# Kernel tuning notes

Hardware: AMD Instinct MI355X
Metric: run time of the kernel (lower is better)

Reference implementation:

```python
import jax, jax.numpy as jnp
import numpy as np
import math

B, S, E, H, D = 2, 2048, 1024, 16, 64

def setup_inputs() -> dict:
    key = jax.random.key(0)
    ks = jax.random.split(key, 9)
    sc = 0.02
    return {
        "x": jax.random.normal(ks[0], (B, S, E), jnp.float32),
        "Wq": jax.random.normal(ks[1], (H, E, D), jnp.float32) * sc,
        "Wk": jax.random.normal(ks[2], (H, E, D), jnp.float32) * sc,
        "Wv": jax.random.normal(ks[3], (H, E, D), jnp.float32) * sc,
        "bq": jax.random.normal(ks[4], (H, D), jnp.float32) * sc,
        "bk": jax.random.normal(ks[5], (H, D), jnp.float32) * sc,
        "bv": jax.random.normal(ks[6], (H, D), jnp.float32) * sc,
        "Wo": jax.random.normal(ks[7], (H * D, E), jnp.float32) * sc,
        "bo": jax.random.normal(ks[8], (E,), jnp.float32) * sc,
    }

def reference(x, Wq, Wk, Wv, bq, bk, bv, Wo, bo):
    # per-head projections, batched over heads: [B,H,S,D]
    q = jnp.einsum('bse,hed->bhsd', x, Wq) + bq[None, :, None, :]
    k = jnp.einsum('bse,hed->bhsd', x, Wk) + bk[None, :, None, :]
    v = jnp.einsum('bse,hed->bhsd', x, Wv) + bv[None, :, None, :]
    # full score matrix [B,H,S,S], scaled by sqrt(head_size) as in original
    scores = jnp.einsum('bhqd,bhkd->bhqk', q, k) / math.sqrt(D)
    causal = jnp.tril(jnp.ones((S, S), bool))  # tril mask as in buffer
    scores = jnp.where(causal[None, None], scores, -jnp.inf)
    attn = jax.nn.softmax(scores, axis=-1)
    out = jnp.einsum('bhqk,bhkd->bhqd', attn, v)
    # concat heads in head order: [B,S,H*D]
    out = out.transpose(0, 2, 1, 3).reshape(B, S, H * D)
    # output projection (dropout is identity in eval / p=0)
    return out @ Wo + bo
```

## Files before the change

### kernel.cpp

```cpp
#include <hip/hip_runtime.h>

#define BB 2
#define SS 2048
#define EE 1024
#define HH 16
#define DD 64

typedef unsigned short u16;
typedef float f4 __attribute__((ext_vector_type(4)));
typedef __bf16 b8 __attribute__((ext_vector_type(8)));
typedef short s8i __attribute__((ext_vector_type(8)));
typedef u16 u16x4 __attribute__((ext_vector_type(4)));

__device__ inline u16 f2b(float f) {
  unsigned u = __builtin_bit_cast(unsigned, f);
  unsigned r = (u + 0x7fffu + ((u >> 16) & 1u)) >> 16;
  return (u16)r;
}

__global__ __launch_bounds__(256) void prep(const float* __restrict__ x,
                                            const float* __restrict__ Wq,
                                            const float* __restrict__ Wk,
                                            const float* __restrict__ Wv,
                                            const float* __restrict__ Wo,
                                            u16* __restrict__ xb,
                                            u16* __restrict__ Wt,
                                            u16* __restrict__ Wot) {
  int bid = blockIdx.x;
  int t = threadIdx.x;
  if (bid < 1024) {
    int i0 = bid * 256 + t;
    for (int j = 0; j < 4; ++j) {
      int i = i0 + j * 262144;
      f4 v = ((const f4*)x)[i];
      u16x4 o;
      for (int k2 = 0; k2 < 4; ++k2) o[k2] = f2b(v[k2]);
      ((u16x4*)xb)[i] = o;
    }
  } else if (bid < 1792) {
    __shared__ float tile[64][65];
    int z = bid - 1024;
    int y = z >> 4;
    int e0 = (z & 15) * 64;
    int qkv = y >> 4, h = y & 15;
    const float* W = (qkv == 0) ? Wq : (qkv == 1) ? Wk : Wv;
    for (int p = 0; p < 16; ++p) {
      int i = p * 4 + (t >> 6), d = t & 63;
      tile[i][d] = W[((size_t)h * EE + e0 + i) * DD + d];
    }
    __syncthreads();
    for (int p = 0; p < 16; ++p) {
      int d = p * 4 + (t >> 6), i = t & 63;
      Wt[((size_t)qkv * 1024 + h * 64 + d) * EE + e0 + i] = f2b(tile[i][d]);
    }
  } else {
    __shared__ float tile2[64][65];
    int z = bid - 1792;
    int e0 = (z & 15) * 64, c0 = (z >> 4) * 64;
    for (int p = 0; p < 16; ++p) {
      int i = p * 4 + (t >> 6), j = t & 63;
      tile2[i][j] = Wo[(size_t)(e0 + i) * (HH * DD) + c0 + j];
    }
    __syncthreads();
    for (int p = 0; p < 16; ++p) {
      int j = p * 4 + (t >> 6), i = t & 63;
      Wot[(size_t)(c0 + j) * EE + e0 + i] = f2b(tile2[i][j]);
    }
  }
}

__global__ __launch_bounds__(256) void gemmQKV(
    const u16* __restrict__ xb, const u16* __restrict__ Wt,
    u16* __restrict__ Qo, u16* __restrict__ Ko, u16* __restrict__ Vo,
    const float* __restrict__ bq, const float* __restrict__ bk,
    const float* __restrict__ bv) {
  const int K = 1024;
  __shared__ u16 SM[8192];
  u16* As = SM;
  u16* Bs = SM + 4096;
  int t = threadIdx.x;
  int lane = t & 63, w = t >> 6;
  int wr = w >> 1, wc = w & 1;
  int lr = lane & 15, lg = lane >> 4;

  int bid = blockIdx.x;
  bool isV = bid >= 512;
  int m0, n0;
  const u16 *Ap, *Bp;
  if (!isV) {
    m0 = (bid >> 4) * 128;
    n0 = (bid & 15) * 128;
    Ap = xb;
    Bp = Wt;
  } else {
    int z = bid - 512;
    m0 = (z >> 5) * 128;
    n0 = (z & 31) * 128;
    Ap = Wt + (size_t)2048 * 1024;
    Bp = xb;
  }

  f4 acc[4][4];
  const f4 z4 = {0.f, 0.f, 0.f, 0.f};
  for (int mi = 0; mi < 4; ++mi)
    for (int ni = 0; ni < 4; ++ni) acc[mi][ni] = z4;

  int r0 = t >> 2, s0 = t & 3;
  const u16* ga0 = Ap + (size_t)(m0 + r0) * K + s0 * 8;
  const u16* gb0 = Bp + (size_t)(n0 + r0) * K + s0 * 8;
  u16* la0 = As + w * 512;
  u16* la1 = As + 2048 + w * 512;
  u16* lb0 = Bs + w * 512;
  u16* lb1 = Bs + 2048 + w * 512;

  for (int ks = 0; ks < K / 32; ++ks) {
    int k0 = ks * 32;
    __builtin_amdgcn_global_load_lds(
        (const __attribute__((address_space(1))) void*)(ga0 + k0),
        (__attribute__((address_space(3))) void*)la0, 16, 0, 0);
    __builtin_amdgcn_global_load_lds(
        (const __attribute__((address_space(1))) void*)(ga0 + 64 * K + k0),
        (__attribute__((address_space(3))) void*)la1, 16, 0, 0);
    __builtin_amdgcn_global_load_lds(
        (const __attribute__((address_space(1))) void*)(gb0 + k0),
        (__attribute__((address_space(3))) void*)lb0, 16, 0, 0);
    __builtin_amdgcn_global_load_lds(
        (const __attribute__((address_space(1))) void*)(gb0 + 64 * K + k0),
        (__attribute__((address_space(3))) void*)lb1, 16, 0, 0);
    __syncthreads();
    b8 af[4], bf[4];
    for (int mi = 0; mi < 4; ++mi)
      af[mi] = *(const b8*)&As[(wr * 64 + mi * 16 + lr) * 32 + lg * 8];
    for (int ni = 0; ni < 4; ++ni)
      bf[ni] = *(const b8*)&Bs[(wc * 64 + ni * 16 + lr) * 32 + lg * 8];
    for (int mi = 0; mi < 4; ++mi)
      for (int ni = 0; ni < 4; ++ni)
        acc[mi][ni] = __builtin_amdgcn_mfma_f32_16x16x32_bf16(af[mi], bf[ni],
                                                              acc[mi][ni], 0, 0, 0);
    __syncthreads();
  }

  const float QSC = 0.18033688011112042f;
  u16(*SMv)[128] = (u16(*)[128])SM;
  for (int hh = 0; hh < 2; ++hh) {
    __syncthreads();
    if (wr == hh) {
      for (int mi = 0; mi < 4; ++mi)
        for (int ni = 0; ni < 4; ++ni)
          for (int r = 0; r < 4; ++r) {
            int lrow = mi * 16 + lg * 4 + r;
            int lcol = wc * 64 + ni * 16 + lr;
            float v = acc[mi][ni][r];
            if (!isV) {
              int n_g = n0 + lcol;
              int qkv = n_g >> 10, hd = n_g & 1023;
              v += (qkv == 0) ? bq[hd] : bk[hd];
              if (qkv == 0) v *= QSC;
            } else {
              v += bv[m0 + hh * 64 + lrow];
            }
            SMv[lrow][lcol] = f2b(v);
          }
    }
    __syncthreads();
    if (!isV) {
      int b = m0 >> 11;
      int sbase = (m0 & 2047) + hh * 64;
      for (int q = 0; q < 4; ++q) {
        int c = t + q * 256;
        int h_i = c >> 9, row = (c >> 3) & 63, slot = c & 7;
        int n_g = n0 + h_i * 64;
        int qkv = n_g >> 10, hd = n_g & 1023;
        int h = hd >> 6;
        u16* dst = (qkv == 0) ? Qo : Ko;
        *(s8i*)(dst + (((size_t)b * HH + h) * SS + sbase + row) * DD + slot * 8) =
            *(const s8i*)&SMv[row][h_i * 64 + slot * 8];
      }
    } else {
      int b = n0 >> 11;
      int scol = n0 & 2047;
      int h = (m0 + hh * 64) >> 6;
      int dbase = (m0 + hh * 64) & 63;
      for (int q = 0; q < 4; ++q) {
        int c = t + q * 256;
        int row = c >> 4, slot = c & 15;
        *(s8i*)(Vo + (((size_t)b * HH + h) * DD + dbase + row) * SS + scol + slot * 8) =
            *(const s8i*)&SMv[row][slot * 8];
      }
    }
  }
}

__global__ __launch_bounds__(256) void gemmO(const u16* __restrict__ A,
                                             const u16* __restrict__ Bm,
                                             float* __restrict__ Co,
                                             const float* __restrict__ bo) {
  const int K = 1024;
  __shared__ u16 As[128 * 32];
  __shared__ u16 Bs[64 * 32];
  __shared__ float Sf[64 * 64];
  int t = threadIdx.x;
  int lane = t & 63, w = t >> 6;
  int lr = lane & 15, lg = lane >> 4;
  int m0 = blockIdx.y * 128, n0 = blockIdx.x * 64;

  f4 acc[2][4];
  const f4 z4 = {0.f, 0.f, 0.f, 0.f};
  for (int mi = 0; mi < 2; ++mi)
    for (int ni = 0; ni < 4; ++ni) acc[mi][ni] = z4;

  int r0 = t >> 2, s0 = t & 3;
  const u16* ga0 = A + (size_t)(m0 + r0) * K + s0 * 8;
  const u16* gb0 = Bm + (size_t)(n0 + r0) * K + s0 * 8;
  u16* la0 = As + w * 512;
  u16* la1 = As + 2048 + w * 512;
  u16* lb0 = Bs + w * 512;

  for (int ks = 0; ks < K / 32; ++ks) {
    int k0 = ks * 32;
    __builtin_amdgcn_global_load_lds(
        (const __attribute__((address_space(1))) void*)(ga0 + k0),
        (__attribute__((address_space(3))) void*)la0, 16, 0, 0);
    __builtin_amdgcn_global_load_lds(
        (const __attribute__((address_space(1))) void*)(ga0 + 64 * K + k0),
        (__attribute__((address_space(3))) void*)la1, 16, 0, 0);
    __builtin_amdgcn_global_load_lds(
        (const __attribute__((address_space(1))) void*)(gb0 + k0),
        (__attribute__((address_space(3))) void*)lb0, 16, 0, 0);
    __syncthreads();
    b8 af[2], bf[4];
    for (int mi = 0; mi < 2; ++mi)
      af[mi] = *(const b8*)&As[(w * 32 + mi * 16 + lr) * 32 + lg * 8];
    for (int ni = 0; ni < 4; ++ni)
      bf[ni] = *(const b8*)&Bs[(ni * 16 + lr) * 32 + lg * 8];
    for (int mi = 0; mi < 2; ++mi)
      for (int ni = 0; ni < 4; ++ni)
        acc[mi][ni] = __builtin_amdgcn_mfma_f32_16x16x32_bf16(af[mi], bf[ni],
                                                              acc[mi][ni], 0, 0, 0);
    __syncthreads();
  }

  for (int hh = 0; hh < 2; ++hh) {
    __syncthreads();
    if ((w >> 1) == hh) {
      for (int mi = 0; mi < 2; ++mi)
        for (int ni = 0; ni < 4; ++ni)
          for (int r = 0; r < 4; ++r) {
            int lrow = (w & 1) * 32 + mi * 16 + lg * 4 + r;
            int lcol = ni * 16 + lr;
            Sf[lrow * 64 + lcol] = acc[mi][ni][r] + bo[n0 + lcol];
          }
    }
    __syncthreads();
    for (int q = 0; q < 4; ++q) {
      int c = t + q * 256;
      int row = c >> 4, slot = c & 15;
      *(f4*)(Co + (size_t)(m0 + hh * 64 + row) * 1024 + n0 + slot * 4) =
          *(const f4*)&Sf[row * 64 + slot * 4];
    }
  }
}

#define KST 72
#define PST 72
__global__ __launch_bounds__(256) void fattn(const u16* __restrict__ Qb,
                                             const u16* __restrict__ Kb,
                                             const u16* __restrict__ VTb,
                                             u16* __restrict__ AO) {
  __shared__ u16 Kl[2][64 * KST];
  __shared__ u16 Vl[2][64 * KST];
  __shared__ u16 Pl[4][16 * PST];

  int t = threadIdx.x, lane = t & 63, w = t >> 6;
  int lr = lane & 15, lg = lane >> 4;
  int bh = blockIdx.y;
  int b = bh >> 4, h = bh & 15;
  size_t base = (size_t)bh * SS * DD;

  int r0 = t >> 2, s0 = t & 3;
  u16* kl0 = &Kl[0][r0 * KST + s0 * 8];
  u16* kl1 = &Kl[1][r0 * KST + s0 * 8];
  u16* vl0 = &Vl[0][r0 * KST + s0 * 8];
  u16* vl1 = &Vl[1][r0 * KST + s0 * 8];
  const u16* kg = Kb + base + (size_t)r0 * DD + s0 * 8;
  const u16* vg = VTb + base + (size_t)r0 * SS + s0 * 8;

  for (int half = 0; half < 2; ++half) {
    int qt = half ? blockIdx.x : 31 - blockIdx.x;
    int qbase = qt * 64;
    int nt = qt + 1;

    const u16* qp = Qb + base + (size_t)(qbase + w * 16 + lr) * DD;
    b8 qf0 = *(const b8*)(qp + lg * 8);
    b8 qf1 = *(const b8*)(qp + 32 + lg * 8);

    const f4 z4 = {0.f, 0.f, 0.f, 0.f};
    f4 o[4];
    for (int i = 0; i < 4; ++i) o[i] = z4;
    float mrow[4], lsum[4];
    for (int r = 0; r < 4; ++r) { mrow[r] = -1e30f; lsum[r] = 0.f; }
    int qg = qbase + w * 16 + lg * 4;

    {
      *(s8i*)kl0 = *(const s8i*)(kg);
      *(s8i*)(kl0 + 32) = *(const s8i*)(kg + 32);
      *(s8i*)vl0 = *(const s8i*)(vg);
      *(s8i*)(vl0 + 32) = *(const s8i*)(vg + 32);
    }
    __syncthreads();

    for (int kt = 0; kt < nt; ++kt) {
      int cur = kt & 1;
      int kv0 = kt * 64;

      s8i nk0, nk1, nv0, nv1;
      bool more = (kt + 1 < nt);
      if (more) {
        const u16* kgn = kg + (size_t)(kv0 + 64) * DD;
        const u16* vgn = vg + kv0 + 64;
        nk0 = *(const s8i*)(kgn);
        nk1 = *(const s8i*)(kgn + 32);
        nv0 = *(const s8i*)(vgn);
        nv1 = *(const s8i*)(vgn + 32);
      }

      f4 sa[4];
      for (int n = 0; n < 4; ++n) sa[n] = z4;
      for (int n = 0; n < 4; ++n) {
        b8 kf0 = *(const b8*)&Kl[cur][(n * 16 + lr) * KST + lg * 8];
        b8 kf1 = *(const b8*)&Kl[cur][(n * 16 + lr) * KST + 32 + lg * 8];
        sa[n] = __builtin_amdgcn_mfma_f32_16x16x32_bf16(qf0, kf0, sa[n], 0, 0, 0);
        sa[n] = __builtin_amdgcn_mfma_f32_16x16x32_bf16(qf1, kf1, sa[n], 0, 0, 0);
      }

      if (kt == nt - 1) {
        for (int r = 0; r < 4; ++r) {
          int q = qg + r;
          if (kv0 + lr > q) sa[0][r] = -1e30f;
          if (kv0 + 16 + lr > q) sa[1][r] = -1e30f;
          if (kv0 + 32 + lr > q) sa[2][r] = -1e30f;
          if (kv0 + 48 + lr > q) sa[3][r] = -1e30f;
        }
      }

      float scl[4];
      for (int r = 0; r < 4; ++r) {
        float mx = fmaxf(fmaxf(sa[0][r], sa[1][r]), fmaxf(sa[2][r], sa[3][r]));
        mx = fmaxf(mx, __shfl_xor(mx, 1));
        mx = fmaxf(mx, __shfl_xor(mx, 2));
        mx = fmaxf(mx, __shfl_xor(mx, 4));
        mx = fmaxf(mx, __shfl_xor(mx, 8));
        float mn = fmaxf(mrow[r], mx);
        float sc = __builtin_amdgcn_exp2f(mrow[r] - mn);
        float p0 = __builtin_amdgcn_exp2f(sa[0][r] - mn);
        float p1 = __builtin_amdgcn_exp2f(sa[1][r] - mn);
        float p2 = __builtin_amdgcn_exp2f(sa[2][r] - mn);
        float p3 = __builtin_amdgcn_exp2f(sa[3][r] - mn);
        lsum[r] = lsum[r] * sc + ((p0 + p1) + (p2 + p3));
        mrow[r] = mn;
        scl[r] = sc;
        int prow = (lg * 4 + r) * PST;
        Pl[w][prow + lr] = f2b(p0);
        Pl[w][prow + 16 + lr] = f2b(p1);
        Pl[w][prow + 32 + lr] = f2b(p2);
        Pl[w][prow + 48 + lr] = f2b(p3);
      }
      for (int n = 0; n < 4; ++n) {
        f4 ov = o[n];
        for (int r = 0; r < 4; ++r) ov[r] *= scl[r];
        o[n] = ov;
      }

      b8 pf0 = *(const b8*)&Pl[w][lr * PST + lg * 8];
      b8 pf1 = *(const b8*)&Pl[w][lr * PST + 32 + lg * 8];
      for (int n = 0; n < 4; ++n) {
        b8 vf0 = *(const b8*)&Vl[cur][(n * 16 + lr) * KST + lg * 8];
        b8 vf1 = *(const b8*)&Vl[cur][(n * 16 + lr) * KST + 32 + lg * 8];
        o[n] = __builtin_amdgcn_mfma_f32_16x16x32_bf16(pf0, vf0, o[n], 0, 0, 0);
        o[n] = __builtin_amdgcn_mfma_f32_16x16x32_bf16(pf1, vf1, o[n], 0, 0, 0);
      }

      if (more) {
        u16* kln = cur ? kl0 : kl1;
        u16* vln = cur ? vl0 : vl1;
        *(s8i*)kln = nk0;
        *(s8i*)(kln + 32) = nk1;
        *(s8i*)vln = nv0;
        *(s8i*)(vln + 32) = nv1;
      }
      __syncthreads();
    }

    float rl[4];
    for (int r = 0; r < 4; ++r) {
      float s = lsum[r];
      s += __shfl_xor(s, 1);
      s += __shfl_xor(s, 2);
      s += __shfl_xor(s, 4);
      s += __shfl_xor(s, 8);
      rl[r] = 1.f / s;
    }
    for (int n = 0; n < 4; ++n)
      for (int r = 0; r < 4; ++r) {
        int qgr = qg + r;
        int d = n * 16 + lr;
        AO[((size_t)b * SS + qgr) * (HH * DD) + h * DD + d] = f2b(o[n][r] * rl[r]);
      }
    __syncthreads();
  }
}

extern "C" void kernel_launch(void* const* d_in, const int* in_sizes, int n_in,
                              void* d_out, int out_size, void* d_ws, size_t ws_size,
                              hipStream_t stream) {
  const float* x  = (const float*)d_in[0];
  const float* Wq = (const float*)d_in[1];
  const float* Wk = (const float*)d_in[2];
  const float* Wv = (const float*)d_in[3];
  const float* bq = (const float*)d_in[4];
  const float* bk = (const float*)d_in[5];
  const float* bv = (const float*)d_in[6];
  const float* Wo = (const float*)d_in[7];
  const float* bo = (const float*)d_in[8];

  char* ws = (char*)d_ws;
  u16* xb  = (u16*)(ws);
  u16* Wt  = (u16*)(ws + ((size_t)8 << 20));
  u16* Wot = (u16*)(ws + ((size_t)14 << 20));
  u16* Qw  = (u16*)(ws + ((size_t)16 << 20));
  u16* Kw  = (u16*)(ws + ((size_t)24 << 20));
  u16* VTw = (u16*)(ws + ((size_t)32 << 20));
  u16* AO  = xb;

  prep<<<2048, 256, 0, stream>>>(x, Wq, Wk, Wv, Wo, xb, Wt, Wot);
  gemmQKV<<<768, 256, 0, stream>>>(xb, Wt, Qw, Kw, VTw, bq, bk, bv);
  fattn<<<dim3(16, 32), 256, 0, stream>>>(Qw, Kw, VTw, AO);
  gemmO<<<dim3(16, 32), 256, 0, stream>>>(AO, Wot, (float*)d_out, bo);
}
```

Measured before the change: 237.6 us.

## Use 128-row query tiles with 8 waves and XOR-swizzled K/V shared layout

The flash-attention kernel now uses 512-thread blocks, each handling one 128-query tile with 8 waves. This replaces the previous 4-wave blocks that processed two paired 64-query tiles in sequence. The grid becomes 1D with head-major ordering, and the largest tiles are scheduled first. K/V staging is spread over twice as many threads with one 16-byte load each and an XOR swizzle on column slots to cut LDS bank conflicts. Each K/V tile load is shared by twice as many query rows, at the cost of fewer blocks and masking on the last two tiles.

```diff
diff --git a/kernel.cpp b/kernel.cpp
--- a/kernel.cpp
+++ b/kernel.cpp
@@ -263,151 +263,143 @@
 
 #define KST 72
 #define PST 72
-__global__ __launch_bounds__(256) void fattn(const u16* __restrict__ Qb,
+__global__ __launch_bounds__(512) void fattn(const u16* __restrict__ Qb,
                                              const u16* __restrict__ Kb,
                                              const u16* __restrict__ VTb,
                                              u16* __restrict__ AO) {
   __shared__ u16 Kl[2][64 * KST];
   __shared__ u16 Vl[2][64 * KST];
-  __shared__ u16 Pl[4][16 * PST];
+  __shared__ u16 Pl[8][16 * PST];
 
   int t = threadIdx.x, lane = t & 63, w = t >> 6;
   int lr = lane & 15, lg = lane >> 4;
-  int bh = blockIdx.y;
+  int id = blockIdx.x;
+  int bh = id & 31;
+  int p = id >> 5;
+  int qb = (p < 8) ? (15 - p) : (p - 8);
   int b = bh >> 4, h = bh & 15;
   size_t base = (size_t)bh * SS * DD;
 
-  int r0 = t >> 2, s0 = t & 3;
-  u16* kl0 = &Kl[0][r0 * KST + s0 * 8];
-  u16* kl1 = &Kl[1][r0 * KST + s0 * 8];
-  u16* vl0 = &Vl[0][r0 * KST + s0 * 8];
-  u16* vl1 = &Vl[1][r0 * KST + s0 * 8];
+  int r0 = t >> 3, s0 = t & 7;
+  int s0p = s0 ^ (r0 & 7);
+  u16* kl0 = &Kl[0][r0 * KST + s0p * 8];
+  u16* kl1 = &Kl[1][r0 * KST + s0p * 8];
+  u16* vl0 = &Vl[0][r0 * KST + s0p * 8];
+  u16* vl1 = &Vl[1][r0 * KST + s0p * 8];
   const u16* kg = Kb + base + (size_t)r0 * DD + s0 * 8;
   const u16* vg = VTb + base + (size_t)r0 * SS + s0 * 8;
 
-  for (int half = 0; half < 2; ++half) {
-    int qt = half ? blockIdx.x : 31 - blockIdx.x;
-    int qbase = qt * 64;
-    int nt = qt + 1;
-
-    const u16* qp = Qb + base + (size_t)(qbase + w * 16 + lr) * DD;
-    b8 qf0 = *(const b8*)(qp + lg * 8);
-    b8 qf1 = *(const b8*)(qp + 32 + lg * 8);
-
-    const f4 z4 = {0.f, 0.f, 0.f, 0.f};
-    f4 o[4];
-    for (int i = 0; i < 4; ++i) o[i] = z4;
-    float mrow[4], lsum[4];
-    for (int r = 0; r < 4; ++r) { mrow[r] = -1e30f; lsum[r] = 0.f; }
-    int qg = qbase + w * 16 + lg * 4;
-
-    {
-      *(s8i*)kl0 = *(const s8i*)(kg);
-      *(s8i*)(kl0 + 32) = *(const s8i*)(kg + 32);
-      *(s8i*)vl0 = *(const s8i*)(vg);
-      *(s8i*)(vl0 + 32) = *(const s8i*)(vg + 32);
-    }
-    __syncthreads();
-
-    for (int kt = 0; kt < nt; ++kt) {
-      int cur = kt & 1;
-      int kv0 = kt * 64;
-
-      s8i nk0, nk1, nv0, nv1;
-      bool more = (kt + 1 < nt);
-      if (more) {
-        const u16* kgn = kg + (size_t)(kv0 + 64) * DD;
-        const u16* vgn = vg + kv0 + 64;
-        nk0 = *(const s8i*)(kgn);
-        nk1 = *(const s8i*)(kgn + 32);
-        nv0 = *(const s8i*)(vgn);
-        nv1 = *(const s8i*)(vgn + 32);
+  int qbase = qb * 128;
+  int nt = 2 * qb + 2;
+
+  const u16* qp = Qb + base + (size_t)(qbase + w * 16 + lr) * DD;
+  b8 qf0 = *(const b8*)(qp + lg * 8);
+  b8 qf1 = *(const b8*)(qp + 32 + lg * 8);
+
+  const f4 z4 = {0.f, 0.f, 0.f, 0.f};
+  f4 o[4];
+  for (int i = 0; i < 4; ++i) o[i] = z4;
+  float mrow[4], lsum[4];
+  for (int r = 0; r < 4; ++r) { mrow[r] = -1e30f; lsum[r] = 0.f; }
+  int qg = qbase + w * 16 + lg * 4;
+
+  int fsl = lg ^ (lr & 7);
+
+  *(s8i*)kl0 = *(const s8i*)kg;
+  *(s8i*)vl0 = *(const s8i*)vg;
+  __syncthreads();
+
+  for (int kt = 0; kt < nt; ++kt) {
+    int cur = kt & 1;
+    int kv0 = kt * 64;
+
+    s8i nk, nv;
+    bool more = (kt + 1 < nt);
+    if (more) {
+      nk = *(const s8i*)(kg + (size_t)(kv0 + 64) * DD);
+      nv = *(const s8i*)(vg + kv0 + 64);
+    }
+
+    f4 sa[4];
+    for (int n = 0; n < 4; ++n) sa[n] = z4;
+    for (int n = 0; n < 4; ++n) {
+      const u16* krow = &Kl[cur][(n * 16 + lr) * KST];
+      b8 kf0 = *(const b8*)(krow + fsl * 8);
+      b8 kf1 = *(const b8*)(krow + (fsl ^ 4) * 8);
+      sa[n] = __builtin_amdgcn_mfma_f32_16x16x32_bf16(qf0, kf0, sa[n], 0, 0, 0);
+      sa[n] = __builtin_amdgcn_mfma_f32_16x16x32_bf16(qf1, kf1, sa[n], 0, 0, 0);
+    }
+
+    if (kt >= nt - 2) {
+      for (int r = 0; r < 4; ++r) {
+        int q = qg + r;
+        if (kv0 + lr > q) sa[0][r] = -1e30f;
+        if (kv0 + 16 + lr > q) sa[1][r] = -1e30f;
+        if (kv0 + 32 + lr > q) sa[2][r] = -1e30f;
+        if (kv0 + 48 + lr > q) sa[3][r] = -1e30f;
       }
-
-      f4 sa[4];
-      for (int n = 0; n < 4; ++n) sa[n] = z4;
-      for (int n = 0; n < 4; ++n) {
-        b8 kf0 = *(const b8*)&Kl[cur][(n * 16 + lr) * KST + lg * 8];
-        b8 kf1 = *(const b8*)&Kl[cur][(n * 16 + lr) * KST + 32 + lg * 8];
-        sa[n] = __builtin_amdgcn_mfma_f32_16x16x32_bf16(qf0, kf0, sa[n], 0, 0, 0);
-        sa[n] = __builtin_amdgcn_mfma_f32_16x16x32_bf16(qf1, kf1, sa[n], 0, 0, 0);
-      }
-
-      if (kt == nt - 1) {
-        for (int r = 0; r < 4; ++r) {
-          int q = qg + r;
-          if (kv0 + lr > q) sa[0][r] = -1e30f;
-          if (kv0 + 16 + lr > q) sa[1][r] = -1e30f;
-          if (kv0 + 32 + lr > q) sa[2][r] = -1e30f;
-          if (kv0 + 48 + lr > q) sa[3][r] = -1e30f;
-        }
-      }
-
-      float scl[4];
-      for (int r = 0; r < 4; ++r) {
-        float mx = fmaxf(fmaxf(sa[0][r], sa[1][r]), fmaxf(sa[2][r], sa[3][r]));
-        mx = fmaxf(mx, __shfl_xor(mx, 1));
-        mx = fmaxf(mx, __shfl_xor(mx, 2));
-        mx = fmaxf(mx, __shfl_xor(mx, 4));
-        mx = fmaxf(mx, __shfl_xor(mx, 8));
-        float mn = fmaxf(mrow[r], mx);
-        float sc = __builtin_amdgcn_exp2f(mrow[r] - mn);
-        float p0 = __builtin_amdgcn_exp2f(sa[0][r] - mn);
-        float p1 = __builtin_amdgcn_exp2f(sa[1][r] - mn);
-        float p2 = __builtin_amdgcn_exp2f(sa[2][r] - mn);
-        float p3 = __builtin_amdgcn_exp2f(sa[3][r] - mn);
-        lsum[r] = lsum[r] * sc + ((p0 + p1) + (p2 + p3));
-        mrow[r] = mn;
-        scl[r] = sc;
-        int prow = (lg * 4 + r) * PST;
-        Pl[w][prow + lr] = f2b(p0);
-        Pl[w][prow + 16 + lr] = f2b(p1);
-        Pl[w][prow + 32 + lr] = f2b(p2);
-        Pl[w][prow + 48 + lr] = f2b(p3);
-      }
-      for (int n = 0; n < 4; ++n) {
-        f4 ov = o[n];
-        for (int r = 0; r < 4; ++r) ov[r] *= scl[r];
-        o[n] = ov;
-      }
-
-      b8 pf0 = *(const b8*)&Pl[w][lr * PST + lg * 8];
-      b8 pf1 = *(const b8*)&Pl[w][lr * PST + 32 + lg * 8];
-      for (int n = 0; n < 4; ++n) {
-        b8 vf0 = *(const b8*)&Vl[cur][(n * 16 + lr) * KST + lg * 8];
-        b8 vf1 = *(const b8*)&Vl[cur][(n * 16 + lr) * KST + 32 + lg * 8];
-        o[n] = __builtin_amdgcn_mfma_f32_16x16x32_bf16(pf0, vf0, o[n], 0, 0, 0);
-        o[n] = __builtin_amdgcn_mfma_f32_16x16x32_bf16(pf1, vf1, o[n], 0, 0, 0);
-      }
-
-      if (more) {
-        u16* kln = cur ? kl0 : kl1;
-        u16* vln = cur ? vl0 : vl1;
-        *(s8i*)kln = nk0;
-        *(s8i*)(kln + 32) = nk1;
-        *(s8i*)vln = nv0;
-        *(s8i*)(vln + 32) = nv1;
-      }
-      __syncthreads();
-    }
-
-    float rl[4];
+    }
+
+    float scl[4];
     for (int r = 0; r < 4; ++r) {
-      float s = lsum[r];
-      s += __shfl_xor(s, 1);
-      s += __shfl_xor(s, 2);
-      s += __shfl_xor(s, 4);
-      s += __shfl_xor(s, 8);
-      rl[r] = 1.f / s;
-    }
-    for (int n = 0; n < 4; ++n)
-      for (int r = 0; r < 4; ++r) {
-        int qgr = qg + r;
-        int d = n * 16 + lr;
-        AO[((size_t)b * SS + qgr) * (HH * DD) + h * DD + d] = f2b(o[n][r] * rl[r]);
-      }
-    __syncthreads();
-  }
+      float mx = fmaxf(fmaxf(sa[0][r], sa[1][r]), fmaxf(sa[2][r], sa[3][r]));
+      mx = fmaxf(mx, __shfl_xor(mx, 1));
+      mx = fmaxf(mx, __shfl_xor(mx, 2));
+      mx = fmaxf(mx, __shfl_xor(mx, 4));
+      mx = fmaxf(mx, __shfl_xor(mx, 8));
+      float mn = fmaxf(mrow[r], mx);
+      float sc = __builtin_amdgcn_exp2f(mrow[r] - mn);
+      float p0 = __builtin_amdgcn_exp2f(sa[0][r] - mn);
+      float p1 = __builtin_amdgcn_exp2f(sa[1][r] - mn);
+      float p2 = __builtin_amdgcn_exp2f(sa[2][r] - mn);
+      float p3 = __builtin_amdgcn_exp2f(sa[3][r] - mn);
+      lsum[r] = lsum[r] * sc + ((p0 + p1) + (p2 + p3));
+      mrow[r] = mn;
+      scl[r] = sc;
+      int prow = (lg * 4 + r) * PST;
+      Pl[w][prow + lr] = f2b(p0);
+      Pl[w][prow + 16 + lr] = f2b(p1);
+      Pl[w][prow + 32 + lr] = f2b(p2);
+      Pl[w][prow + 48 + lr] = f2b(p3);
+    }
+    for (int n = 0; n < 4; ++n) {
+      f4 ov = o[n];
+      for (int r = 0; r < 4; ++r) ov[r] *= scl[r];
+      o[n] = ov;
+    }
+
+    b8 pf0 = *(const b8*)&Pl[w][lr * PST + lg * 8];
+    b8 pf1 = *(const b8*)&Pl[w][lr * PST + 32 + lg * 8];
+    for (int n = 0; n < 4; ++n) {
+      const u16* vrow = &Vl[cur][(n * 16 + lr) * KST];
+      b8 vf0 = *(const b8*)(vrow + fsl * 8);
+      b8 vf1 = *(const b8*)(vrow + (fsl ^ 4) * 8);
+      o[n] = __builtin_amdgcn_mfma_f32_16x16x32_bf16(pf0, vf0, o[n], 0, 0, 0);
+      o[n] = __builtin_amdgcn_mfma_f32_16x16x32_bf16(pf1, vf1, o[n], 0, 0, 0);
+    }
+
+    if (more) {
+      *(s8i*)(cur ? kl0 : kl1) = nk;
+      *(s8i*)(cur ? vl0 : vl1) = nv;
+    }
+    __syncthreads();
+  }
+
+  float rl[4];
+  for (int r = 0; r < 4; ++r) {
+    float s = lsum[r];
+    s += __shfl_xor(s, 1);
+    s += __shfl_xor(s, 2);
+    s += __shfl_xor(s, 4);
+    s += __shfl_xor(s, 8);
+    rl[r] = 1.f / s;
+  }
+  for (int n = 0; n < 4; ++n)
+    for (int r = 0; r < 4; ++r) {
+      int qgr = qg + r;
+      int d = n * 16 + lr;
+      AO[((size_t)b * SS + qgr) * (HH * DD) + h * DD + d] = f2b(o[n][r] * rl[r]);
+    }
 }
 
 extern "C" void kernel_launch(void* const* d_in, const int* in_sizes, int n_in,
@@ -434,6 +426,6 @@
 
   prep<<<2048, 256, 0, stream>>>(x, Wq, Wk, Wv, Wo, xb, Wt, Wot);
   gemmQKV<<<768, 256, 0, stream>>>(xb, Wt, Qw, Kw, VTw, bq, bk, bv);
-  fattn<<<dim3(16, 32), 256, 0, stream>>>(Qw, Kw, VTw, AO);
+  fattn<<<512, 512, 0, stream>>>(Qw, Kw, VTw, AO);
   gemmO<<<dim3(16, 32), 256, 0, stream>>>(AO, Wot, (float*)d_out, bo);
 }
```

Result: no change. 235.7 us (-0.8%).
